# Kernel optimization log

Hardware: AMD Instinct MI355X
Metric: run time of the kernel (lower is better)

Reference implementation:

```python
import jax, jax.numpy as jnp
import numpy as np

D = 1024       # embedding_dim
H = 4096       # mlp_dim
E = 64         # num_experts
K = 3          # top-k
B, S = 2, 2048
C = 512


def setup_inputs() -> dict:
    key = jax.random.key(0)
    ks = jax.random.split(key, 6)
    s = 0.02
    return {
        "x": jax.random.normal(ks[0], (B, S, D), jnp.float32),
        "gate_w": jax.random.normal(ks[1], (D, E), jnp.float32) * s,
        "gate_b": jnp.zeros((E,), jnp.float32),
        "w1": jax.random.normal(ks[2], (E, D, H), jnp.float32) * s,
        "b1": jnp.zeros((E, H), jnp.float32),
        "w2": jax.random.normal(ks[3], (E, H, D), jnp.float32) * s,
        "b2": jnp.zeros((E, D), jnp.float32),
    }


def reference(x, gate_w, gate_b, w1, b1, w2, b2):
    xf = x.reshape(-1, D)                       # [T, D] flattened tokens
    T = xf.shape[0]
    # --- top-k gating (eval mode: clean logits, no noise) ---
    logits = xf @ gate_w + gate_b               # [T, E]
    top_l, top_i = jax.lax.top_k(logits, K)     # [T, K]
    gates = jax.nn.softmax(top_l, axis=-1)      # softmax over the k selected logits
    # --- token permutation / dispatch (capacity-based, order-preserving) ---
    fe = top_i.reshape(-1)                      # [T*K] expert id per assignment
    fg = gates.reshape(-1)                      # [T*K] gate per assignment
    tok = jnp.repeat(jnp.arange(T), K)          # [T*K] source token id
    oh = jax.nn.one_hot(fe, E, dtype=jnp.int32) # [T*K, E]
    pos = (jnp.cumsum(oh, axis=0) * oh).sum(-1) - 1  # slot within expert buffer
    valid = pos < C                             # capacity mask (C sized so nothing drops in practice)
    # scatter tokens into per-expert buffers; OOB (pos>=C) rows dropped
    buf = jnp.zeros((E, C, D), x.dtype).at[fe, pos].set(xf[tok], mode='drop')
    # --- grouped expert MLP: Linear -> exact GELU -> Linear ---
    h = jax.nn.gelu(jnp.einsum('ecd,edh->ech', buf, w1) + b1[:, None, :], approximate=False)
    y = jnp.einsum('ech,ehd->ecd', h, w2) + b2[:, None, :]  # [E, C, D]
    # --- gather back, gate, scatter-add combine ---
    rows = y[fe, jnp.minimum(pos, C - 1)] * (fg * valid.astype(x.dtype))[:, None]
    out = jnp.zeros_like(xf).at[tok].add(rows)
    return out.reshape(x.shape)
```

## Files before the change

### kernel.cpp

```cpp
#include <hip/hip_runtime.h>

#define TTOK 4096
#define DDIM 1024
#define HDIM 4096
#define NEXP 64
#define CAP  512
#define NASN (TTOK*3)

typedef unsigned short u16;
typedef __attribute__((ext_vector_type(8))) short s16x8;
typedef __attribute__((ext_vector_type(4))) short s16x4;
typedef __attribute__((ext_vector_type(4))) float f32x4;

__device__ __forceinline__ u16 f2bf(float f) {
  union { float f; unsigned u; } v; v.f = f;
  unsigned u = v.u;
  return (u16)((u + 0x7fffu + ((u >> 16) & 1u)) >> 16);
}

__device__ __forceinline__ void gl_lds16(const void* g, void* l) {
  __builtin_amdgcn_global_load_lds(
      (const __attribute__((address_space(1))) void*)g,
      (__attribute__((address_space(3))) void*)l, 16, 0, 0);
}

__global__ __launch_bounds__(512) void gate_topk(
    const float* __restrict__ x, const float* __restrict__ gw,
    const float* __restrict__ gb, int* __restrict__ fe, float* __restrict__ fg)
{
  int lane = threadIdx.x & 63;
  int wid  = threadIdx.x >> 6;
  int t = blockIdx.x * 8 + wid;
  const float* xr = x + (size_t)t * DDIM;
  float acc = gb[lane];
  #pragma unroll 4
  for (int d = 0; d < DDIM; d++) acc += xr[d] * gw[d * NEXP + lane];

  float v = acc;
  float bv[3]; int bi[3];
  #pragma unroll
  for (int j = 0; j < 3; j++) {
    float mv = v; int mi = lane;
    #pragma unroll
    for (int off = 32; off; off >>= 1) {
      float ov = __shfl_xor(mv, off);
      int   oi = __shfl_xor(mi, off);
      if (ov > mv || (ov == mv && oi < mi)) { mv = ov; mi = oi; }
    }
    bv[j] = mv; bi[j] = mi;
    if (lane == mi) v = -3.4e38f;
  }
  if (lane == 0) {
    float e1 = expf(bv[1] - bv[0]), e2 = expf(bv[2] - bv[0]);
    float inv = 1.0f / (1.0f + e1 + e2);
    fe[t*3+0] = bi[0]; fe[t*3+1] = bi[1]; fe[t*3+2] = bi[2];
    fg[t*3+0] = inv;   fg[t*3+1] = e1*inv; fg[t*3+2] = e2*inv;
  }
}

__global__ __launch_bounds__(64) void scan_pos(
    const int* __restrict__ fe, int* __restrict__ posA,
    int* __restrict__ s2a, int* __restrict__ cnt)
{
  int e = blockIdx.x, lane = threadIdx.x;
  int base = 0;
  for (int i0 = 0; i0 < NASN; i0 += 64) {
    int i = i0 + lane;
    bool m = (fe[i] == e);
    unsigned long long bal = __ballot(m);
    int below = __popcll(bal & ((1ull << lane) - 1ull));
    if (m) {
      int p = base + below;
      posA[i] = p;
      if (p < CAP) s2a[e * CAP + p] = i;
    }
    base += __popcll(bal);
  }
  if (lane == 0) cnt[e] = base < CAP ? base : CAP;
}

__global__ __launch_bounds__(64) void dispatch(
    const float* __restrict__ x, const int* __restrict__ fe,
    const int* __restrict__ posA, u16* __restrict__ bufA)
{
  int a = blockIdx.x;
  int p = posA[a];
  if (p >= CAP) return;
  int e = fe[a];
  int tok = a / 3;
  int l = threadIdx.x;
  const float4* xr = (const float4*)(x + (size_t)tok * DDIM);
  u16* dst = bufA + ((size_t)e * CAP + p) * DDIM;
  #pragma unroll
  for (int j = 0; j < 4; j++) {
    float4 v = xr[j * 64 + l];
    uint2 u;
    u.x = (unsigned)f2bf(v.x) | ((unsigned)f2bf(v.y) << 16);
    u.y = (unsigned)f2bf(v.z) | ((unsigned)f2bf(v.w) << 16);
    *(uint2*)(dst + (size_t)(j * 64 + l) * 4) = u;
  }
}

__global__ __launch_bounds__(256) void combine(
    const float* __restrict__ y, const int* __restrict__ fe,
    const float* __restrict__ fg, const int* __restrict__ posA,
    float* __restrict__ out)
{
  int t = blockIdx.x;
  int d4 = threadIdx.x;
  float4 s = (float4){0.f, 0.f, 0.f, 0.f};
  #pragma unroll
  for (int k = 0; k < 3; k++) {
    int a = t * 3 + k;
    int p = posA[a];
    if (p < CAP) {
      float g = fg[a];
      float4 v = *(const float4*)(y + ((size_t)fe[a] * CAP + p) * DDIM + d4 * 4);
      s.x += g * v.x; s.y += g * v.y; s.z += g * v.z; s.w += g * v.w;
    }
  }
  *(float4*)(out + (size_t)t * DDIM + d4 * 4) = s;
}

template<int KTOT, int NTOT, int EPI>
__global__ __launch_bounds__(256, 2) void moe_gemm(
    const u16* __restrict__ Abuf, const float* __restrict__ W,
    const float* __restrict__ bias, u16* __restrict__ hout,
    float* __restrict__ yout, const int* __restrict__ cnt, int g0)
{
  constexpr int NCT = NTOT / 128;
  constexpr int NT  = KTOT / 64;
  int NB = gridDim.x;
  int b = blockIdx.x;
  int L = (b & 7) * (NB >> 3) + (b >> 3);
  int tcol = L % NCT;
  int rt   = (L / NCT) & 1;
  int el   = L / (NCT * 2);
  int e    = g0 + el;
  int cnte = cnt[e];
  int c0   = rt * 256;
  if (c0 >= cnte) return;
  int n0 = tcol * 128;

  int tid = threadIdx.x, l = tid & 63, w = tid >> 6;

  __shared__ char AsB[256 * 128];
  __shared__ char BsB[128 * 136];

  const u16* Arows = Abuf + ((size_t)((EPI == 1 ? e : el)) * CAP + c0) * (size_t)KTOT;
  const float* We = W + (size_t)e * KTOT * NTOT;

  int bn4 = tid & 31, bkb = (tid >> 5) * 8;
  const float* Wt = We + (size_t)bkb * NTOT + n0 + bn4 * 4;
  char* BsW = BsB + (bn4 * 4) * 136 + bkb * 2;

  float4 brB4[8];
  #define LOADB(t) { \
    const float* p_ = Wt + (size_t)(t) * 64 * NTOT; \
    _Pragma("unroll") \
    for (int j_ = 0; j_ < 8; j_++) \
      brB4[j_] = *(const float4*)(p_ + (size_t)j_ * NTOT); \
    }
  #define STOREB() { \
    _Pragma("unroll") \
    for (int c_ = 0; c_ < 4; c_++) { \
      float v0_ = (c_==0?brB4[0].x:c_==1?brB4[0].y:c_==2?brB4[0].z:brB4[0].w); \
      float v1_ = (c_==0?brB4[1].x:c_==1?brB4[1].y:c_==2?brB4[1].z:brB4[1].w); \
      float v2_ = (c_==0?brB4[2].x:c_==1?brB4[2].y:c_==2?brB4[2].z:brB4[2].w); \
      float v3_ = (c_==0?brB4[3].x:c_==1?brB4[3].y:c_==2?brB4[3].z:brB4[3].w); \
      float v4_ = (c_==0?brB4[4].x:c_==1?brB4[4].y:c_==2?brB4[4].z:brB4[4].w); \
      float v5_ = (c_==0?brB4[5].x:c_==1?brB4[5].y:c_==2?brB4[5].z:brB4[5].w); \
      float v6_ = (c_==0?brB4[6].x:c_==1?brB4[6].y:c_==2?brB4[6].z:brB4[6].w); \
      float v7_ = (c_==0?brB4[7].x:c_==1?brB4[7].y:c_==2?brB4[7].z:brB4[7].w); \
      uint2 ua_, ub_; \
      ua_.x = (unsigned)f2bf(v0_) | ((unsigned)f2bf(v1_) << 16); \
      ua_.y = (unsigned)f2bf(v2_) | ((unsigned)f2bf(v3_) << 16); \
      ub_.x = (unsigned)f2bf(v4_) | ((unsigned)f2bf(v5_) << 16); \
      ub_.y = (unsigned)f2bf(v6_) | ((unsigned)f2bf(v7_) << 16); \
      *(uint2*)(BsW + c_ * 136) = ua_; \
      *(uint2*)(BsW + c_ * 136 + 8) = ub_; \
    } }

  f32x4 acc[4][8];
  #pragma unroll
  for (int m = 0; m < 4; m++)
    #pragma unroll
    for (int nn = 0; nn < 8; nn++)
      acc[m][nn] = (f32x4){0.f, 0.f, 0.f, 0.f};

  LOADB(0);

  for (int t = 0; t < NT; ++t) {
    #pragma unroll
    for (int i = 0; i < 8; i++) {
      int r = i * 32 + w * 8 + (l >> 3);
      int cswz = (l & 7) ^ (r & 7);
      const char* gsrc = (const char*)(Arows + (size_t)r * KTOT + (size_t)t * 64) + cswz * 16;
      gl_lds16(gsrc, AsB + (i * 32 + w * 8) * 128);
    }
    STOREB();
    __builtin_amdgcn_sched_barrier(0);
    if (t + 1 < NT) {
      LOADB(t + 1);
      __builtin_amdgcn_sched_barrier(0);
      asm volatile("s_waitcnt vmcnt(8)" ::: "memory");
    } else {
      asm volatile("s_waitcnt vmcnt(0)" ::: "memory");
    }
    asm volatile("s_waitcnt lgkmcnt(0)" ::: "memory");
    __builtin_amdgcn_sched_barrier(0);
    __builtin_amdgcn_s_barrier();
    __builtin_amdgcn_sched_barrier(0);

    #pragma unroll
    for (int k2 = 0; k2 < 2; k2++) {
      int kb = k2 * 32;
      s16x8 af[4], bf8[8];
      #pragma unroll
      for (int m = 0; m < 4; m++) {
        int R = w * 64 + m * 16 + (l & 15);
        int chunk = (kb >> 3) + (l >> 4);
        int sc = chunk ^ (R & 7);
        af[m] = *(const s16x8*)(AsB + R * 128 + sc * 16);
      }
      #pragma unroll
      for (int nn = 0; nn < 8; nn++) {
        int Nn = nn * 16 + (l & 15);
        int kk = kb + (l >> 4) * 8;
        const char* bp = BsB + Nn * 136 + kk * 2;
        union { s16x8 v8; s16x4 v4[2]; } bu;
        bu.v4[0] = *(const s16x4*)bp;
        bu.v4[1] = *(const s16x4*)(bp + 8);
        bf8[nn] = bu.v8;
      }
      #pragma unroll
      for (int m = 0; m < 4; m++)
        #pragma unroll
        for (int nn = 0; nn < 8; nn++)
          acc[m][nn] = __builtin_amdgcn_mfma_f32_16x16x32_bf16(af[m], bf8[nn], acc[m][nn], 0, 0, 0);
    }
    __builtin_amdgcn_s_barrier();
    __builtin_amdgcn_sched_barrier(0);
  }

  int lr = l >> 4, lc = l & 15;
  float bv[8];
  #pragma unroll
  for (int nn = 0; nn < 8; nn++) bv[nn] = bias[(size_t)e * NTOT + n0 + nn * 16 + lc];

  if (EPI == 1) {
    #pragma unroll
    for (int m = 0; m < 4; m++)
      #pragma unroll
      for (int q = 0; q < 4; q++) {
        int rowL = w * 64 + m * 16 + lr * 4 + q;
        if (c0 + rowL < cnte) {
          #pragma unroll
          for (int nn = 0; nn < 8; nn++) {
            float vv = acc[m][nn][q] + bv[nn];
            vv = 0.5f * vv * (1.0f + erff(vv * 0.70710678118f));
            hout[(size_t)(el * CAP + c0 + rowL) * NTOT + (n0 + nn * 16 + lc)] = f2bf(vv);
          }
        }
      }
  } else {
    #pragma unroll
    for (int m = 0; m < 4; m++) {
      int rowbase = w * 64 + m * 16 + lr * 4;
      #pragma unroll
      for (int q = 0; q < 4; q++) {
        int slot = c0 + rowbase + q;
        if (slot < cnte) {
          float* yr = yout + ((size_t)e * CAP + slot) * DDIM + n0;
          #pragma unroll
          for (int nn = 0; nn < 8; nn++)
            yr[nn * 16 + lc] = acc[m][nn][q] + bv[nn];
        }
      }
    }
  }
}

extern "C" void kernel_launch(void* const* d_in, const int* in_sizes, int n_in,
                              void* d_out, int out_size, void* d_ws, size_t ws_size,
                              hipStream_t stream) {
  (void)in_sizes; (void)n_in; (void)ws_size; (void)out_size;
  const float* x  = (const float*)d_in[0];
  const float* gw = (const float*)d_in[1];
  const float* gb = (const float*)d_in[2];
  const float* w1 = (const float*)d_in[3];
  const float* b1 = (const float*)d_in[4];
  const float* w2 = (const float*)d_in[5];
  const float* b2 = (const float*)d_in[6];
  float* out = (float*)d_out;

  char* ws = (char*)d_ws;
  int*   fe   = (int*)(ws);
  float* fg   = (float*)(ws + 49152);
  int*   posA = (int*)(ws + 98304);
  int*   s2a  = (int*)(ws + 147456);
  int*   cnt  = (int*)(ws + 278528);
  u16*   bufA = (u16*)(ws + (1 << 20));
  u16*   hbuf = (u16*)(ws + (1 << 20) + 67108864ull);
  float* ybuf = (float*)(ws + (1 << 20) + 67108864ull + 268435456ull);

  gate_topk<<<TTOK / 8, 512, 0, stream>>>(x, gw, gb, fe, fg);
  scan_pos<<<NEXP, 64, 0, stream>>>(fe, posA, s2a, cnt);
  dispatch<<<NASN, 64, 0, stream>>>(x, fe, posA, bufA);

  moe_gemm<DDIM, HDIM, 1><<<NEXP * 2 * (HDIM / 128), 256, 0, stream>>>(
      bufA, w1, b1, hbuf, nullptr, cnt, 0);
  moe_gemm<HDIM, DDIM, 2><<<NEXP * 2 * (DDIM / 128), 256, 0, stream>>>(
      hbuf, w2, b2, nullptr, ybuf, cnt, 0);

  combine<<<TTOK, 256, 0, stream>>>(ybuf, fe, fg, posA, out);
}
```

Measured before the change: 692.3 us.

## Prefetch next A tile into wave-private LDS rows during MFMA compute

The A-tile global-to-LDS row mapping is remapped so each wave loads exactly the 64 rows it later reads. The load of the next k-tile's A is then issued mid-iteration, after the wave has read its second-half A fragments, instead of at the top of the loop. This is meant to overlap A-tile global latency with the second half of the MFMA work. Correctness relies on the lgkmcnt wait and on wave-private ownership of the A rows. The vmcnt accounting is unchanged in structure.

```diff
diff --git a/kernel.cpp b/kernel.cpp
--- a/kernel.cpp
+++ b/kernel.cpp
@@ -181,6 +181,18 @@
       *(uint2*)(BsW + c_ * 136 + 8) = ub_; \
     } }
 
+  #define GLDS_A(t) { \
+    _Pragma("unroll") \
+    for (int i_ = 0; i_ < 8; i_++) { \
+      int rb_ = w * 64 + i_ * 8; \
+      int r_  = rb_ + (l >> 3); \
+      int cswz_ = (l & 7) ^ (r_ & 7); \
+      const char* gsrc_ = (const char*)(Arows + (size_t)r_ * KTOT + (size_t)(t) * 64) + cswz_ * 16; \
+      gl_lds16(gsrc_, AsB + rb_ * 128); \
+    } }
+
+  #define SB() __builtin_amdgcn_sched_barrier(0)
+
   f32x4 acc[4][8];
   #pragma unroll
   for (int m = 0; m < 4; m++)
@@ -188,45 +200,36 @@
     for (int nn = 0; nn < 8; nn++)
       acc[m][nn] = (f32x4){0.f, 0.f, 0.f, 0.f};
 
+  GLDS_A(0);
   LOADB(0);
 
   for (int t = 0; t < NT; ++t) {
-    #pragma unroll
-    for (int i = 0; i < 8; i++) {
-      int r = i * 32 + w * 8 + (l >> 3);
-      int cswz = (l & 7) ^ (r & 7);
-      const char* gsrc = (const char*)(Arows + (size_t)r * KTOT + (size_t)t * 64) + cswz * 16;
-      gl_lds16(gsrc, AsB + (i * 32 + w * 8) * 128);
-    }
     STOREB();
-    __builtin_amdgcn_sched_barrier(0);
+    SB();
     if (t + 1 < NT) {
       LOADB(t + 1);
-      __builtin_amdgcn_sched_barrier(0);
+      SB();
       asm volatile("s_waitcnt vmcnt(8)" ::: "memory");
     } else {
       asm volatile("s_waitcnt vmcnt(0)" ::: "memory");
     }
     asm volatile("s_waitcnt lgkmcnt(0)" ::: "memory");
-    __builtin_amdgcn_sched_barrier(0);
+    SB();
     __builtin_amdgcn_s_barrier();
-    __builtin_amdgcn_sched_barrier(0);
-
-    #pragma unroll
-    for (int k2 = 0; k2 < 2; k2++) {
-      int kb = k2 * 32;
+    SB();
+
+    {
       s16x8 af[4], bf8[8];
       #pragma unroll
       for (int m = 0; m < 4; m++) {
         int R = w * 64 + m * 16 + (l & 15);
-        int chunk = (kb >> 3) + (l >> 4);
-        int sc = chunk ^ (R & 7);
+        int sc = (l >> 4) ^ (R & 7);
         af[m] = *(const s16x8*)(AsB + R * 128 + sc * 16);
       }
       #pragma unroll
       for (int nn = 0; nn < 8; nn++) {
         int Nn = nn * 16 + (l & 15);
-        int kk = kb + (l >> 4) * 8;
+        int kk = (l >> 4) * 8;
         const char* bp = BsB + Nn * 136 + kk * 2;
         union { s16x8 v8; s16x4 v4[2]; } bu;
         bu.v4[0] = *(const s16x4*)bp;
@@ -238,9 +241,35 @@
         #pragma unroll
         for (int nn = 0; nn < 8; nn++)
           acc[m][nn] = __builtin_amdgcn_mfma_f32_16x16x32_bf16(af[m], bf8[nn], acc[m][nn], 0, 0, 0);
+
+      #pragma unroll
+      for (int m = 0; m < 4; m++) {
+        int R = w * 64 + m * 16 + (l & 15);
+        int sc = (4 + (l >> 4)) ^ (R & 7);
+        af[m] = *(const s16x8*)(AsB + R * 128 + sc * 16);
+      }
+      if (t + 1 < NT) {
+        asm volatile("s_waitcnt lgkmcnt(0)" ::: "memory");
+        GLDS_A(t + 1);
+      }
+      #pragma unroll
+      for (int nn = 0; nn < 8; nn++) {
+        int Nn = nn * 16 + (l & 15);
+        int kk = 32 + (l >> 4) * 8;
+        const char* bp = BsB + Nn * 136 + kk * 2;
+        union { s16x8 v8; s16x4 v4[2]; } bu;
+        bu.v4[0] = *(const s16x4*)bp;
+        bu.v4[1] = *(const s16x4*)(bp + 8);
+        bf8[nn] = bu.v8;
+      }
+      #pragma unroll
+      for (int m = 0; m < 4; m++)
+        #pragma unroll
+        for (int nn = 0; nn < 8; nn++)
+          acc[m][nn] = __builtin_amdgcn_mfma_f32_16x16x32_bf16(af[m], bf8[nn], acc[m][nn], 0, 0, 0);
     }
     __builtin_amdgcn_s_barrier();
-    __builtin_amdgcn_sched_barrier(0);
+    SB();
   }
 
   int lr = l >> 4, lc = l & 15;
```

New measurement: 671.9 us. 1.03x faster.
